# Performance work log

Hardware: AMD Instinct MI355X
Metric: run time of the kernel (lower is better)

Reference implementation:

```python
import jax, jax.numpy as jnp
import numpy as np

EPS = 1e-6
MAX_ITER = 3

def skew(w):
    z = jnp.zeros_like(w[:, 0])
    return jnp.stack([
        jnp.stack([z, -w[:, 2], w[:, 1]], -1),
        jnp.stack([w[:, 2], z, -w[:, 0]], -1),
        jnp.stack([-w[:, 1], w[:, 0], z], -1)], -2)

def twist2mat(w):
    # Rodrigues formula, w: [B,3] -> R: [B,3,3]
    theta = jnp.linalg.norm(w, axis=-1, keepdims=True) + 1e-12
    axis = w / theta
    Km = skew(axis)
    th = theta[..., None]
    I = jnp.eye(3, dtype=w.dtype)
    return I + jnp.sin(th) * Km + (1.0 - jnp.cos(th)) * (Km @ Km)

def sobel_gradient(img, normalize=True):
    # replicate-pad + 3x3 Sobel, img: [B,C,H,W]
    p = jnp.pad(img, ((0, 0), (0, 0), (1, 1), (1, 1)), mode='edge')
    tl = p[..., :-2, :-2]; tc = p[..., :-2, 1:-1]; tr = p[..., :-2, 2:]
    ml = p[..., 1:-1, :-2]; mr = p[..., 1:-1, 2:]
    bl = p[..., 2:, :-2]; bc = p[..., 2:, 1:-1]; br = p[..., 2:, 2:]
    dx = (tr - tl) + 2.0 * (mr - ml) + (br - bl)
    dy = (bl - tl) + 2.0 * (bc - tc) + (br - tr)
    if normalize:
        mag = jnp.sqrt(dx * dx + dy * dy + 1e-8)
        dx, dy = dx / mag, dy / mag
    return dx, dy

def _bilinear_one(F, u, v):
    # F: [C,H,W]; u,v: [H,W] pixel coords; border padding (grid_sample-like)
    C, H, W = F.shape
    u = jnp.clip(u, 0.0, W - 1.0)
    v = jnp.clip(v, 0.0, H - 1.0)
    x0 = jnp.floor(u); y0 = jnp.floor(v)
    wx = u - x0; wy = v - y0
    x0i = x0.astype(jnp.int32); y0i = y0.astype(jnp.int32)
    x1i = jnp.minimum(x0i + 1, W - 1); y1i = jnp.minimum(y0i + 1, H - 1)
    g = lambda yi, xi: F[:, yi, xi]  # advanced-index gather -> [C,H,W]
    return (g(y0i, x0i) * (1 - wx) * (1 - wy) + g(y0i, x1i) * wx * (1 - wy)
            + g(y1i, x0i) * (1 - wx) * wy + g(y1i, x1i) * wx * wy)

def warp_features(F, u, v):
    # F: [B,C,H,W]; u,v: [B,1,H,W]
    return jax.vmap(_bilinear_one)(F, u[:, 0], v[:, 0])

def generate_xy_grid(B, H, W, K):
    fx, fy, cx, cy = [K[:, i].reshape(B, 1, 1, 1) for i in range(4)]
    uu, vv = jnp.meshgrid(jnp.arange(W, dtype=K.dtype), jnp.arange(H, dtype=K.dtype))
    px = (uu[None, None] - cx) / fx
    py = (vv[None, None] - cy) / fy
    return px, py  # [B,1,H,W] each

def batch_warp_inverse_depth(px, py, invD0, R, t, K):
    B, _, H, W = px.shape
    xy1 = jnp.concatenate([px, py, jnp.ones_like(px)], 1).reshape(B, 3, -1)
    warped = R @ xy1 + t[:, :, None] * invD0.reshape(B, 1, -1)
    x_, y_, s_ = warped[:, 0], warped[:, 1], warped[:, 2]
    fx, fy, cx, cy = [K[:, i].reshape(B, 1) for i in range(4)]
    u_ = (x_ / s_ * fx + cx).reshape(B, 1, H, W)
    v_ = (y_ / s_ * fy + cy).reshape(B, 1, H, W)
    inv_z = invD0 / s_.reshape(B, 1, H, W)
    return u_, v_, inv_z

def check_occ(inv_z_buffer, invD1, u, v, thres=0.1):
    B, _, H, W = invD1.shape
    inv_z_warped = warp_features(invD1, u, v)
    inlier = inv_z_buffer > inv_z_warped - thres
    inview = (u > 0) & (u < W) & (v > 0) & (v < H)
    return ~(inlier & inview)  # [B,1,H,W] bool

def compute_jacobian_warping(invD, K, px, py):
    # linearized at origin (pose=None branch)
    B, _, H, W = invD.shape
    x = px.reshape(B, -1); y = py.reshape(B, -1); d = invD.reshape(B, -1)
    O = jnp.zeros_like(x)
    xy = x * y
    dx_dp = jnp.stack([-xy, 1.0 + x * x, -y, d, O, -d * x], -1)
    dy_dp = jnp.stack([-(1.0 + y * y), xy, x, O, d, -d * y], -1)
    fx = K[:, 0].reshape(B, 1, 1); fy = K[:, 1].reshape(B, 1, 1)
    return dx_dp * fx, dy_dp * fy  # [B,HW,6] each

def lev_mar_H(JtWJ):
    diag = jnp.eye(6, dtype=JtWJ.dtype)
    trace = jnp.trace(JtWJ, axis1=1, axis2=2)
    return JtWJ + (trace * 1e-6)[:, None, None] * diag

def forward(twist0, x0, x1, invD0, invD1, sigma0, sigma1, K):
    B, C, H, W = x0.shape
    N = H * W
    dtype = x0.dtype
    R = twist2mat(twist0[:, :3])
    t = twist0[:, 3:]
    px, py = generate_xy_grid(B, H, W, K)
    # inverse-compositional: template Jacobian precomputed once
    Jf_x, Jf_y = sobel_gradient(x0, normalize=True)
    Jx_p, Jy_p = compute_jacobian_warping(invD0, K, px, py)
    J = (Jf_x.reshape(B, C, N, 1) * Jx_p.reshape(B, 1, N, 6)
         + Jf_y.reshape(B, C, N, 1) * Jy_p.reshape(B, 1, N, 6))  # [B,C,N,6]
    for _ in range(MAX_ITER):
        u_w, v_w, inv_z = batch_warp_inverse_depth(px, py, invD0, R, t, K)
        occ = check_occ(inv_z, invD1, u_w, v_w)
        f_r = warp_features(x1, u_w, v_w)
        sigma_r = warp_features(sigma1, u_w, v_w)
        res = f_r - x0
        sigma = jnp.sqrt(sigma_r * sigma_r + sigma0 * sigma0)
        wres = jnp.where(occ, EPS, res / sigma)  # [B,C,H,W]
        valid = (~occ).reshape(B, 1, N, 1).astype(dtype)
        Jw = (J / sigma.reshape(B, C, N, 1) * valid).reshape(B, C * N, 6)
        r = jnp.where(occ, 0.0, wres).reshape(B, C * N)
        JtWJ = jnp.einsum('bnk,bnl->bkl', Jw, Jw)
        Rhs = jnp.einsum('bnk,bn->bk', Jw, r)[..., None]
        xi = jnp.linalg.solve(lev_mar_H(JtWJ), Rhs)  # [B,6,1]
        d_R = twist2mat(-xi[:, :3, 0])
        d_t = -(d_R @ xi[:, 3:])
        t = (R @ d_t)[:, :, 0] + t
        R = R @ d_R
    return jnp.concatenate([R.reshape(B, 9), t], axis=1)  # [B,12]

def setup_inputs() -> dict:
    key = jax.random.key(0)
    ks = jax.random.split(key, 7)
    B, C, H, W = 8, 16, 240, 320
    twist0 = jax.random.normal(ks[0], (B, 6), jnp.float32) * 0.01
    x0 = jax.random.normal(ks[1], (B, C, H, W), jnp.float32)
    x1 = jax.random.normal(ks[2], (B, C, H, W), jnp.float32)
    invD0 = jax.random.uniform(ks[3], (B, 1, H, W), jnp.float32, 0.1, 1.0)
    invD1 = jax.random.uniform(ks[4], (B, 1, H, W), jnp.float32, 0.1, 1.0)
    sigma0 = jax.random.uniform(ks[5], (B, C, H, W), jnp.float32, 0.1, 1.0)
    sigma1 = jax.random.uniform(ks[6], (B, C, H, W), jnp.float32, 0.1, 1.0)
    Kmat = jnp.tile(jnp.array([[0.8 * W, 0.8 * W, W / 2.0, H / 2.0]], jnp.float32), (B, 1))
    return dict(twist0=twist0, x0=x0, x1=x1, invD0=invD0, invD1=invD1,
                sigma0=sigma0, sigma1=sigma1, K=Kmat)

def reference(twist0, x0, x1, invD0, invD1, sigma0, sigma1, K):
    return forward(twist0, x0, x1, invD0, invD1, sigma0, sigma1, K)
```

## Files before the change

kernel.cpp:

```cpp
#include <hip/hip_runtime.h>
#include <hip/hip_fp16.h>

#define B_ 8
#define C_ 16
#define H_ 240
#define W_ 320
#define N_ (H_*W_)

__device__ __forceinline__ void twist2mat_dev(float w0, float w1, float w2, float R[9]) {
    float th = sqrtf(w0*w0 + w1*w1 + w2*w2) + 1e-12f;
    float ax = w0/th, ay = w1/th, az = w2/th;
    float s = sinf(th), c = cosf(th), ic = 1.0f - c;
    R[0] = 1.0f + ic*(ax*ax - 1.0f);
    R[1] = -s*az + ic*ax*ay;
    R[2] =  s*ay + ic*ax*az;
    R[3] =  s*az + ic*ax*ay;
    R[4] = 1.0f + ic*(ay*ay - 1.0f);
    R[5] = -s*ax + ic*ay*az;
    R[6] = -s*ay + ic*ax*az;
    R[7] =  s*ax + ic*ay*az;
    R[8] = 1.0f + ic*(az*az - 1.0f);
}

__device__ __forceinline__ unsigned pack_h2(float a, float b) {
    __half2 h = __floats2half2_rn(a, b);
    return *reinterpret_cast<unsigned*>(&h);
}
__device__ __forceinline__ float2 unpack_h2(unsigned u) {
    __half2 h = *reinterpret_cast<__half2*>(&u);
    return __half22float2(h);
}

__device__ __forceinline__ void solve_update(const float* __restrict__ ac, float R[9], float t[3]) {
    float M[6][7];
    {
        int idx = 0;
        #pragma unroll
        for (int k = 0; k < 6; k++)
            #pragma unroll
            for (int l = k; l < 6; l++) { M[k][l] = ac[idx]; M[l][k] = ac[idx]; idx++; }
    }
    const float trace = M[0][0]+M[1][1]+M[2][2]+M[3][3]+M[4][4]+M[5][5];
    const float lam = trace * 1e-6f;
    #pragma unroll
    for (int i = 0; i < 6; i++) { M[i][i] += lam; M[i][6] = ac[21+i]; }

    #pragma unroll
    for (int k = 0; k < 6; k++) {
        const float inv = 1.0f / M[k][k];
        #pragma unroll
        for (int i = k+1; i < 6; i++) {
            const float f = M[i][k] * inv;
            #pragma unroll
            for (int j = k; j < 7; j++) M[i][j] -= f * M[k][j];
        }
    }
    float xi[6];
    #pragma unroll
    for (int i = 5; i >= 0; i--) {
        float s = M[i][6];
        #pragma unroll
        for (int j = i+1; j < 6; j++) s -= M[i][j]*xi[j];
        xi[i] = s / M[i][i];
    }

    float dR[9];
    twist2mat_dev(-xi[0], -xi[1], -xi[2], dR);
    const float dt0 = -(dR[0]*xi[3] + dR[1]*xi[4] + dR[2]*xi[5]);
    const float dt1 = -(dR[3]*xi[3] + dR[4]*xi[4] + dR[5]*xi[5]);
    const float dt2 = -(dR[6]*xi[3] + dR[7]*xi[4] + dR[8]*xi[5]);

    const float nt0 = R[0]*dt0 + R[1]*dt1 + R[2]*dt2 + t[0];
    const float nt1 = R[3]*dt0 + R[4]*dt1 + R[5]*dt2 + t[1];
    const float nt2 = R[6]*dt0 + R[7]*dt1 + R[8]*dt2 + t[2];
    float nR[9];
    #pragma unroll
    for (int i = 0; i < 3; i++)
        #pragma unroll
        for (int j = 0; j < 3; j++)
            nR[i*3+j] = R[i*3+0]*dR[0*3+j] + R[i*3+1]*dR[1*3+j] + R[i*3+2]*dR[2*3+j];
    #pragma unroll
    for (int i = 0; i < 9; i++) R[i] = nR[i];
    t[0] = nt0; t[1] = nt1; t[2] = nt2;
}

__device__ __forceinline__ void build_RT(const float* __restrict__ twist0,
                                         const float* __restrict__ accum,
                                         int b, int iters, float R[9], float t[3]) {
    const float* w = twist0 + b*6;
    twist2mat_dev(w[0], w[1], w[2], R);
    t[0] = w[3]; t[1] = w[4]; t[2] = w[5];
    for (int j = 0; j < iters; j++)
        solve_update(accum + (size_t)(j*B_ + b)*27, R, t);
}

__launch_bounds__(256)
__global__ void precompute_kernel(const float* __restrict__ x0, const float* __restrict__ x1,
                                  const float* __restrict__ sigma0, const float* __restrict__ sigma1,
                                  uint4* __restrict__ P0h, uint4* __restrict__ X1S1h,
                                  float* __restrict__ accum)
{
    if (blockIdx.x == 0 && blockIdx.y == 0 && blockIdx.z == 0) {
        for (int k = threadIdx.x; k < 3*B_*27; k += 256) accum[k] = 0.0f;
    }
    const int pix = blockIdx.x*256 + threadIdx.x;
    const int cg = blockIdx.y;
    const int b = blockIdx.z;
    const int h = pix / W_, w = pix - h*W_;
    const int hm = max(h-1,0), hp = min(h+1,H_-1);
    const int wm = max(w-1,0), wp = min(w+1,W_-1);

    unsigned p0[8];
    unsigned xsp[4];
    #pragma unroll
    for (int i = 0; i < 4; i++) {
        const int c = cg*4 + i;
        const size_t base = ((size_t)(b*C_+c))*N_;
        const float* xc = x0 + base;
        const float tl = xc[hm*W_+wm], tc_ = xc[hm*W_+w], tr = xc[hm*W_+wp];
        const float ml = xc[h*W_+wm],                     mr = xc[h*W_+wp];
        const float bl = xc[hp*W_+wm], bc_ = xc[hp*W_+w], br = xc[hp*W_+wp];
        const float dx = tr - tl + 2.0f*(mr - ml) + (br - bl);
        const float dy = bl - tl + 2.0f*(bc_ - tc_) + (br - tr);
        const float mag = sqrtf(dx*dx + dy*dy + 1e-8f);
        const float s0v = sigma0[base + pix];
        p0[i*2+0] = pack_h2(dx/mag, dy/mag);
        p0[i*2+1] = pack_h2(xc[pix], s0v*s0v);
        xsp[i] = pack_h2(x1[base + pix], sigma1[base + pix]);
    }
    uint4 a; a.x = p0[0]; a.y = p0[1]; a.z = p0[2]; a.w = p0[3];
    uint4 bb; bb.x = p0[4]; bb.y = p0[5]; bb.z = p0[6]; bb.w = p0[7];
    P0h[((size_t)(b*8 + cg*2  ))*N_ + pix] = a;
    P0h[((size_t)(b*8 + cg*2+1))*N_ + pix] = bb;
    uint4 q; q.x = xsp[0]; q.y = xsp[1]; q.z = xsp[2]; q.w = xsp[3];
    X1S1h[((size_t)(b*4 + cg))*N_ + pix] = q;
}

__launch_bounds__(256)
__global__ void iter_kernel(const uint4* __restrict__ P0h, const uint4* __restrict__ X1S1h,
                            const float* __restrict__ invD0, const float* __restrict__ invD1,
                            const float* __restrict__ Kmat, const float* __restrict__ twist0,
                            float* __restrict__ accum, int it)
{
    const int b = blockIdx.y;
    const int pix = blockIdx.x * 256 + threadIdx.x;
    const int h = pix / W_;
    const int w = pix - h*W_;

    float Rm[9], tv[3];
    build_RT(twist0, accum, b, it, Rm, tv);

    const float fx = Kmat[b*4+0], fy = Kmat[b*4+1], cx = Kmat[b*4+2], cy = Kmat[b*4+3];

    float acc[27];
    #pragma unroll
    for (int j = 0; j < 27; j++) acc[j] = 0.0f;

    const float px = ((float)w - cx) / fx;
    const float py = ((float)h - cy) / fy;
    const float d  = invD0[b*N_ + pix];

    const float x_ = Rm[0]*px + Rm[1]*py + Rm[2] + tv[0]*d;
    const float y_ = Rm[3]*px + Rm[4]*py + Rm[5] + tv[1]*d;
    const float s_ = Rm[6]*px + Rm[7]*py + Rm[8] + tv[2]*d;
    const float u = x_/s_*fx + cx;
    const float v = y_/s_*fy + cy;
    const float inv_z = d / s_;

    const float uc = fminf(fmaxf(u, 0.0f), (float)(W_-1));
    const float vc = fminf(fmaxf(v, 0.0f), (float)(H_-1));
    const float x0f = floorf(uc), y0f = floorf(vc);
    const float wx = uc - x0f, wy = vc - y0f;
    const int x0i = (int)x0f, y0i = (int)y0f;
    const int x1i = min(x0i+1, W_-1), y1i = min(y0i+1, H_-1);
    const float w00 = (1.0f-wx)*(1.0f-wy), w01 = wx*(1.0f-wy);
    const float w10 = (1.0f-wx)*wy,        w11 = wx*wy;
    const int i00 = y0i*W_+x0i, i01 = y0i*W_+x1i, i10 = y1i*W_+x0i, i11 = y1i*W_+x1i;

    const float* dz = invD1 + b*N_;
    const float zw = dz[i00]*w00 + dz[i01]*w01 + dz[i10]*w10 + dz[i11]*w11;
    const bool inlier = inv_z > zw - 0.1f;
    const bool inview = (u > 0.0f) && (u < (float)W_) && (v > 0.0f) && (v < (float)H_);
    const bool valid  = inlier && inview;

    if (valid) {
        const float xy = px*py;
        const float Av[6] = { -xy*fx, (1.0f+px*px)*fx, -py*fx, d*fx, 0.0f, -d*px*fx };
        const float Bv[6] = { -(1.0f+py*py)*fy, xy*fy, px*fy, 0.0f, d*fy, -d*py*fy };

        float Swxx=0.f, Swxy=0.f, Swyy=0.f, Srx=0.f, Sry=0.f;
        const uint4* P0b   = P0h   + (size_t)b*8*N_;
        const uint4* X1S1b = X1S1h + (size_t)b*4*N_;

#define CH(gword, xword, t00, t01, t10, t11) { \
        const float2 g  = unpack_h2(gword); \
        const float2 xs = unpack_h2(xword); \
        const float2 a00 = unpack_h2(t00), a01 = unpack_h2(t01), \
                     a10 = unpack_h2(t10), a11 = unpack_h2(t11); \
        const float fr = a00.x*w00 + a01.x*w01 + a10.x*w10 + a11.x*w11; \
        const float sr = a00.y*w00 + a01.y*w01 + a10.y*w10 + a11.y*w11; \
        const float inv_s2 = 1.0f/(sr*sr + xs.y); \
        const float res = fr - xs.x; \
        const float gxw = g.x*inv_s2, gyw = g.y*inv_s2; \
        Swxx += g.x*gxw; Swxy += g.x*gyw; Swyy += g.y*gyw; \
        Srx  += res*gxw; Sry  += res*gyw; }

        #pragma unroll
        for (int cg = 0; cg < 4; cg++) {
            const uint4 pA = P0b[(size_t)(cg*2  )*N_ + pix];
            const uint4 pB = P0b[(size_t)(cg*2+1)*N_ + pix];
            const uint4* xsb = X1S1b + (size_t)cg*N_;
            const uint4 q00 = xsb[i00], q01 = xsb[i01], q10 = xsb[i10], q11 = xsb[i11];
            CH(pA.x, pA.y, q00.x, q01.x, q10.x, q11.x)
            CH(pA.z, pA.w, q00.y, q01.y, q10.y, q11.y)
            CH(pB.x, pB.y, q00.z, q01.z, q10.z, q11.z)
            CH(pB.z, pB.w, q00.w, q01.w, q10.w, q11.w)
        }
#undef CH

        int idx = 0;
        #pragma unroll
        for (int k = 0; k < 6; k++) {
            #pragma unroll
            for (int l = k; l < 6; l++) {
                acc[idx++] = Swxx*Av[k]*Av[l] + Swxy*(Av[k]*Bv[l] + Bv[k]*Av[l]) + Swyy*Bv[k]*Bv[l];
            }
        }
        #pragma unroll
        for (int k = 0; k < 6; k++) acc[21+k] = Srx*Av[k] + Sry*Bv[k];
    }

    const int lane = threadIdx.x & 63;
    const int wave = threadIdx.x >> 6;
    __shared__ float red[4][27];
    #pragma unroll
    for (int j = 0; j < 27; j++) {
        float vv = acc[j];
        vv += __shfl_down(vv, 32);
        vv += __shfl_down(vv, 16);
        vv += __shfl_down(vv, 8);
        vv += __shfl_down(vv, 4);
        vv += __shfl_down(vv, 2);
        vv += __shfl_down(vv, 1);
        if (lane == 0) red[wave][j] = vv;
    }
    __syncthreads();
    if (threadIdx.x < 27) {
        float s = red[0][threadIdx.x] + red[1][threadIdx.x] + red[2][threadIdx.x] + red[3][threadIdx.x];
        atomicAdd(&accum[(size_t)(it*B_ + b)*27 + threadIdx.x], s);
    }
}

__global__ void finalize_kernel(const float* __restrict__ twist0, const float* __restrict__ accum,
                                float* __restrict__ out)
{
    const int b = threadIdx.x;
    if (b >= B_) return;
    float Rm[9], tv[3];
    build_RT(twist0, accum, b, 3, Rm, tv);
    float* ob = out + b*12;
    #pragma unroll
    for (int i = 0; i < 9; i++) ob[i] = Rm[i];
    ob[9] = tv[0]; ob[10] = tv[1]; ob[11] = tv[2];
}

extern "C" void kernel_launch(void* const* d_in, const int* in_sizes, int n_in,
                              void* d_out, int out_size, void* d_ws, size_t ws_size,
                              hipStream_t stream) {
    const float* twist0 = (const float*)d_in[0];
    const float* x0     = (const float*)d_in[1];
    const float* x1     = (const float*)d_in[2];
    const float* invD0  = (const float*)d_in[3];
    const float* invD1  = (const float*)d_in[4];
    const float* sigma0 = (const float*)d_in[5];
    const float* sigma1 = (const float*)d_in[6];
    const float* Kmat   = (const float*)d_in[7];
    float* out = (float*)d_out;

    const size_t p0_bytes = (size_t)B_*8*N_*sizeof(uint4);
    const size_t xs_bytes = (size_t)B_*4*N_*sizeof(uint4);

    uint4* P0h   = (uint4*)d_ws;
    uint4* X1S1h = (uint4*)((char*)d_ws + p0_bytes);
    float* accum = (float*)((char*)d_ws + p0_bytes + xs_bytes);

    hipLaunchKernelGGL(precompute_kernel, dim3(N_/256, 4, B_), dim3(256), 0, stream,
                       x0, x1, sigma0, sigma1, P0h, X1S1h, accum);

    dim3 grid(N_/256, B_);
    for (int it = 0; it < 3; ++it) {
        hipLaunchKernelGGL(iter_kernel, grid, dim3(256), 0, stream,
                           P0h, X1S1h, invD0, invD1, Kmat, twist0, accum, it);
    }
    hipLaunchKernelGGL(finalize_kernel, dim3(1), dim3(64), 0, stream, twist0, accum, out);
}
```

Before: 366.8 us.

## Process four pixels per thread in precompute and two per thread in iterations

The precompute kernel now handles four consecutive pixels per thread. It uses float4 row loads and shares the Sobel stencil neighbours across those pixels, which cuts redundant scalar global loads. The iteration kernel has each thread accumulate two pixels, halving the block count and the per-block work of rebuilding R/t and running the 27-value reduction and atomics. This raises per-thread register pressure and lowers the number of threads available to hide gather latency.

```diff
diff --git a/kernel.cpp b/kernel.cpp
--- a/kernel.cpp
+++ b/kernel.cpp
@@ -103,62 +103,71 @@
     if (blockIdx.x == 0 && blockIdx.y == 0 && blockIdx.z == 0) {
         for (int k = threadIdx.x; k < 3*B_*27; k += 256) accum[k] = 0.0f;
     }
-    const int pix = blockIdx.x*256 + threadIdx.x;
+    const int p4 = blockIdx.x*256 + threadIdx.x;
+    const int pix = p4 * 4;
     const int cg = blockIdx.y;
-    const int b = blockIdx.z;
-    const int h = pix / W_, w = pix - h*W_;
+    const int b  = blockIdx.z;
+    const int h = pix / W_;
+    const int w = pix - h*W_;
     const int hm = max(h-1,0), hp = min(h+1,H_-1);
-    const int wm = max(w-1,0), wp = min(w+1,W_-1);
-
-    unsigned p0[8];
-    unsigned xsp[4];
+    const int wl = max(w-1,0), wr = min(w+4,W_-1);
+
+    unsigned gw[4][4], xw[4][4], qw[4][4];
+
     #pragma unroll
     for (int i = 0; i < 4; i++) {
         const int c = cg*4 + i;
         const size_t base = ((size_t)(b*C_+c))*N_;
         const float* xc = x0 + base;
-        const float tl = xc[hm*W_+wm], tc_ = xc[hm*W_+w], tr = xc[hm*W_+wp];
-        const float ml = xc[h*W_+wm],                     mr = xc[h*W_+wp];
-        const float bl = xc[hp*W_+wm], bc_ = xc[hp*W_+w], br = xc[hp*W_+wp];
-        const float dx = tr - tl + 2.0f*(mr - ml) + (br - bl);
-        const float dy = bl - tl + 2.0f*(bc_ - tc_) + (br - tr);
-        const float mag = sqrtf(dx*dx + dy*dy + 1e-8f);
-        const float s0v = sigma0[base + pix];
-        p0[i*2+0] = pack_h2(dx/mag, dy/mag);
-        p0[i*2+1] = pack_h2(xc[pix], s0v*s0v);
-        xsp[i] = pack_h2(x1[base + pix], sigma1[base + pix]);
-    }
-    uint4 a; a.x = p0[0]; a.y = p0[1]; a.z = p0[2]; a.w = p0[3];
-    uint4 bb; bb.x = p0[4]; bb.y = p0[5]; bb.z = p0[6]; bb.w = p0[7];
-    P0h[((size_t)(b*8 + cg*2  ))*N_ + pix] = a;
-    P0h[((size_t)(b*8 + cg*2+1))*N_ + pix] = bb;
-    uint4 q; q.x = xsp[0]; q.y = xsp[1]; q.z = xsp[2]; q.w = xsp[3];
-    X1S1h[((size_t)(b*4 + cg))*N_ + pix] = q;
-}
-
-__launch_bounds__(256)
-__global__ void iter_kernel(const uint4* __restrict__ P0h, const uint4* __restrict__ X1S1h,
-                            const float* __restrict__ invD0, const float* __restrict__ invD1,
-                            const float* __restrict__ Kmat, const float* __restrict__ twist0,
-                            float* __restrict__ accum, int it)
+        const float4 rt = *reinterpret_cast<const float4*>(xc + hm*W_ + w);
+        const float4 rm = *reinterpret_cast<const float4*>(xc + h *W_ + w);
+        const float4 rb = *reinterpret_cast<const float4*>(xc + hp*W_ + w);
+        const float T[6]  = { xc[hm*W_+wl], rt.x, rt.y, rt.z, rt.w, xc[hm*W_+wr] };
+        const float Mw[6] = { xc[h *W_+wl], rm.x, rm.y, rm.z, rm.w, xc[h *W_+wr] };
+        const float Bo[6] = { xc[hp*W_+wl], rb.x, rb.y, rb.z, rb.w, xc[hp*W_+wr] };
+        const float4 s0v = *reinterpret_cast<const float4*>(sigma0 + base + pix);
+        const float4 x1v = *reinterpret_cast<const float4*>(x1 + base + pix);
+        const float4 s1v = *reinterpret_cast<const float4*>(sigma1 + base + pix);
+        const float s0a[4] = {s0v.x, s0v.y, s0v.z, s0v.w};
+        const float x1a[4] = {x1v.x, x1v.y, x1v.z, x1v.w};
+        const float s1a[4] = {s1v.x, s1v.y, s1v.z, s1v.w};
+        #pragma unroll
+        for (int j = 0; j < 4; j++) {
+            const float dx = T[j+2] - T[j] + 2.0f*(Mw[j+2] - Mw[j]) + (Bo[j+2] - Bo[j]);
+            const float dy = Bo[j] - T[j] + 2.0f*(Bo[j+1] - T[j+1]) + (Bo[j+2] - T[j+2]);
+            const float mag = sqrtf(dx*dx + dy*dy + 1e-8f);
+            gw[i][j] = pack_h2(dx/mag, dy/mag);
+            xw[i][j] = pack_h2(Mw[j+1], s0a[j]*s0a[j]);
+            qw[i][j] = pack_h2(x1a[j], s1a[j]);
+        }
+    }
+    uint4* PA = P0h + ((size_t)(b*8 + cg*2  ))*N_ + pix;
+    uint4* PB = P0h + ((size_t)(b*8 + cg*2+1))*N_ + pix;
+    uint4* Qp = X1S1h + ((size_t)(b*4 + cg))*N_ + pix;
+    #pragma unroll
+    for (int j = 0; j < 4; j++) {
+        uint4 a;  a.x = gw[0][j];  a.y = xw[0][j];  a.z = gw[1][j];  a.w = xw[1][j];
+        uint4 bb; bb.x = gw[2][j]; bb.y = xw[2][j]; bb.z = gw[3][j]; bb.w = xw[3][j];
+        uint4 q;  q.x = qw[0][j];  q.y = qw[1][j];  q.z = qw[2][j];  q.w = qw[3][j];
+        PA[j] = a; PB[j] = bb; Qp[j] = q;
+    }
+}
+
+__device__ __forceinline__ void accum_pixel(int pix,
+                                            const float Rm[9], const float tv[3],
+                                            float fx, float fy, float cx, float cy,
+                                            const uint4* __restrict__ P0b,
+                                            const uint4* __restrict__ X1S1b,
+                                            const float* __restrict__ d0,
+                                            const float* __restrict__ dz,
+                                            float* __restrict__ acc)
 {
-    const int b = blockIdx.y;
-    const int pix = blockIdx.x * 256 + threadIdx.x;
     const int h = pix / W_;
     const int w = pix - h*W_;
 
-    float Rm[9], tv[3];
-    build_RT(twist0, accum, b, it, Rm, tv);
-
-    const float fx = Kmat[b*4+0], fy = Kmat[b*4+1], cx = Kmat[b*4+2], cy = Kmat[b*4+3];
-
-    float acc[27];
-    #pragma unroll
-    for (int j = 0; j < 27; j++) acc[j] = 0.0f;
-
     const float px = ((float)w - cx) / fx;
     const float py = ((float)h - cy) / fy;
-    const float d  = invD0[b*N_ + pix];
+    const float d  = d0[pix];
 
     const float x_ = Rm[0]*px + Rm[1]*py + Rm[2] + tv[0]*d;
     const float y_ = Rm[3]*px + Rm[4]*py + Rm[5] + tv[1]*d;
@@ -177,58 +186,82 @@
     const float w10 = (1.0f-wx)*wy,        w11 = wx*wy;
     const int i00 = y0i*W_+x0i, i01 = y0i*W_+x1i, i10 = y1i*W_+x0i, i11 = y1i*W_+x1i;
 
-    const float* dz = invD1 + b*N_;
     const float zw = dz[i00]*w00 + dz[i01]*w01 + dz[i10]*w10 + dz[i11]*w11;
     const bool inlier = inv_z > zw - 0.1f;
     const bool inview = (u > 0.0f) && (u < (float)W_) && (v > 0.0f) && (v < (float)H_);
     const bool valid  = inlier && inview;
 
-    if (valid) {
-        const float xy = px*py;
-        const float Av[6] = { -xy*fx, (1.0f+px*px)*fx, -py*fx, d*fx, 0.0f, -d*px*fx };
-        const float Bv[6] = { -(1.0f+py*py)*fy, xy*fy, px*fy, 0.0f, d*fy, -d*py*fy };
-
-        float Swxx=0.f, Swxy=0.f, Swyy=0.f, Srx=0.f, Sry=0.f;
-        const uint4* P0b   = P0h   + (size_t)b*8*N_;
-        const uint4* X1S1b = X1S1h + (size_t)b*4*N_;
+    if (!valid) return;
+
+    const float xy = px*py;
+    const float Av[6] = { -xy*fx, (1.0f+px*px)*fx, -py*fx, d*fx, 0.0f, -d*px*fx };
+    const float Bv[6] = { -(1.0f+py*py)*fy, xy*fy, px*fy, 0.0f, d*fy, -d*py*fy };
+
+    float Swxx=0.f, Swxy=0.f, Swyy=0.f, Srx=0.f, Sry=0.f;
 
 #define CH(gword, xword, t00, t01, t10, t11) { \
-        const float2 g  = unpack_h2(gword); \
-        const float2 xs = unpack_h2(xword); \
-        const float2 a00 = unpack_h2(t00), a01 = unpack_h2(t01), \
-                     a10 = unpack_h2(t10), a11 = unpack_h2(t11); \
-        const float fr = a00.x*w00 + a01.x*w01 + a10.x*w10 + a11.x*w11; \
-        const float sr = a00.y*w00 + a01.y*w01 + a10.y*w10 + a11.y*w11; \
-        const float inv_s2 = 1.0f/(sr*sr + xs.y); \
-        const float res = fr - xs.x; \
-        const float gxw = g.x*inv_s2, gyw = g.y*inv_s2; \
-        Swxx += g.x*gxw; Swxy += g.x*gyw; Swyy += g.y*gyw; \
-        Srx  += res*gxw; Sry  += res*gyw; }
-
-        #pragma unroll
-        for (int cg = 0; cg < 4; cg++) {
-            const uint4 pA = P0b[(size_t)(cg*2  )*N_ + pix];
-            const uint4 pB = P0b[(size_t)(cg*2+1)*N_ + pix];
-            const uint4* xsb = X1S1b + (size_t)cg*N_;
-            const uint4 q00 = xsb[i00], q01 = xsb[i01], q10 = xsb[i10], q11 = xsb[i11];
-            CH(pA.x, pA.y, q00.x, q01.x, q10.x, q11.x)
-            CH(pA.z, pA.w, q00.y, q01.y, q10.y, q11.y)
-            CH(pB.x, pB.y, q00.z, q01.z, q10.z, q11.z)
-            CH(pB.z, pB.w, q00.w, q01.w, q10.w, q11.w)
+    const float2 g  = unpack_h2(gword); \
+    const float2 xs = unpack_h2(xword); \
+    const float2 a00 = unpack_h2(t00), a01 = unpack_h2(t01), \
+                 a10 = unpack_h2(t10), a11 = unpack_h2(t11); \
+    const float fr = a00.x*w00 + a01.x*w01 + a10.x*w10 + a11.x*w11; \
+    const float sr = a00.y*w00 + a01.y*w01 + a10.y*w10 + a11.y*w11; \
+    const float inv_s2 = 1.0f/(sr*sr + xs.y); \
+    const float res = fr - xs.x; \
+    const float gxw = g.x*inv_s2, gyw = g.y*inv_s2; \
+    Swxx += g.x*gxw; Swxy += g.x*gyw; Swyy += g.y*gyw; \
+    Srx  += res*gxw; Sry  += res*gyw; }
+
+    #pragma unroll
+    for (int cg = 0; cg < 4; cg++) {
+        const uint4 pA = P0b[(size_t)(cg*2  )*N_ + pix];
+        const uint4 pB = P0b[(size_t)(cg*2+1)*N_ + pix];
+        const uint4* xsb = X1S1b + (size_t)cg*N_;
+        const uint4 q00 = xsb[i00], q01 = xsb[i01], q10 = xsb[i10], q11 = xsb[i11];
+        CH(pA.x, pA.y, q00.x, q01.x, q10.x, q11.x)
+        CH(pA.z, pA.w, q00.y, q01.y, q10.y, q11.y)
+        CH(pB.x, pB.y, q00.z, q01.z, q10.z, q11.z)
+        CH(pB.z, pB.w, q00.w, q01.w, q10.w, q11.w)
+    }
+#undef CH
+
+    int idx = 0;
+    #pragma unroll
+    for (int k = 0; k < 6; k++) {
+        #pragma unroll
+        for (int l = k; l < 6; l++) {
+            acc[idx++] += Swxx*Av[k]*Av[l] + Swxy*(Av[k]*Bv[l] + Bv[k]*Av[l]) + Swyy*Bv[k]*Bv[l];
         }
-#undef CH
-
-        int idx = 0;
-        #pragma unroll
-        for (int k = 0; k < 6; k++) {
-            #pragma unroll
-            for (int l = k; l < 6; l++) {
-                acc[idx++] = Swxx*Av[k]*Av[l] + Swxy*(Av[k]*Bv[l] + Bv[k]*Av[l]) + Swyy*Bv[k]*Bv[l];
-            }
-        }
-        #pragma unroll
-        for (int k = 0; k < 6; k++) acc[21+k] = Srx*Av[k] + Sry*Bv[k];
-    }
+    }
+    #pragma unroll
+    for (int k = 0; k < 6; k++) acc[21+k] += Srx*Av[k] + Sry*Bv[k];
+}
+
+__launch_bounds__(256)
+__global__ void iter_kernel(const uint4* __restrict__ P0h, const uint4* __restrict__ X1S1h,
+                            const float* __restrict__ invD0, const float* __restrict__ invD1,
+                            const float* __restrict__ Kmat, const float* __restrict__ twist0,
+                            float* __restrict__ accum, int it)
+{
+    const int b = blockIdx.y;
+    const int pix0 = blockIdx.x * 512 + threadIdx.x;
+
+    float Rm[9], tv[3];
+    build_RT(twist0, accum, b, it, Rm, tv);
+
+    const float fx = Kmat[b*4+0], fy = Kmat[b*4+1], cx = Kmat[b*4+2], cy = Kmat[b*4+3];
+
+    float acc[27];
+    #pragma unroll
+    for (int j = 0; j < 27; j++) acc[j] = 0.0f;
+
+    const uint4* P0b   = P0h   + (size_t)b*8*N_;
+    const uint4* X1S1b = X1S1h + (size_t)b*4*N_;
+    const float* d0 = invD0 + b*N_;
+    const float* dz = invD1 + b*N_;
+
+    accum_pixel(pix0,       Rm, tv, fx, fy, cx, cy, P0b, X1S1b, d0, dz, acc);
+    accum_pixel(pix0 + 256, Rm, tv, fx, fy, cx, cy, P0b, X1S1b, d0, dz, acc);
 
     const int lane = threadIdx.x & 63;
     const int wave = threadIdx.x >> 6;
@@ -284,10 +317,10 @@
     uint4* X1S1h = (uint4*)((char*)d_ws + p0_bytes);
     float* accum = (float*)((char*)d_ws + p0_bytes + xs_bytes);
 
-    hipLaunchKernelGGL(precompute_kernel, dim3(N_/256, 4, B_), dim3(256), 0, stream,
+    hipLaunchKernelGGL(precompute_kernel, dim3(N_/(256*4), 4, B_), dim3(256), 0, stream,
                        x0, x1, sigma0, sigma1, P0h, X1S1h, accum);
 
-    dim3 grid(N_/256, B_);
+    dim3 grid(N_/512, B_);
     for (int it = 0; it < 3; ++it) {
         hipLaunchKernelGGL(iter_kernel, grid, dim3(256), 0, stream,
                            P0h, X1S1h, invD0, invD1, Kmat, twist0, accum, it);
```

Result: no change. 363.9 us (-0.8%).
